# Kernel tuning notes

Hardware: AMD Instinct MI355X
Metric: run time of the kernel (lower is better)

The kernel has to match this reference:

```python
import jax, jax.numpy as jnp
import numpy as np

N = 50000        # n_nodes
E = 1600000      # n_edges (avg degree 32)
M = 8            # multiplicity of node irreps 8x0e + 8x1o
R = 8            # radial embedding dim
H = 8            # radial MLP hidden width
OUT_IRREPS = 6 * M   # 24x0e + 24x1o -> 48 irreps (MLP output width)
AVG_NEIGH = 32.0
SQRT3 = np.sqrt(3.0).astype(np.float32)


def setup_inputs() -> dict:
    key = jax.random.key(0)
    ks = jax.random.split(key, 7)
    node_feats = jax.random.normal(ks[0], (N, 4 * M), dtype=jnp.float32)      # [M scalars | M*3 vector comps]
    edge_features = jax.random.normal(ks[1], (E, 4), dtype=jnp.float32)       # SH l=0 (1) + l=1 (3)
    radial_embedding = jax.random.uniform(ks[2], (E, R), dtype=jnp.float32)
    senders = jax.random.randint(ks[3], (E,), 0, N, dtype=jnp.int32)
    receivers = jax.random.randint(ks[4], (E,), 0, N, dtype=jnp.int32)
    w1 = jax.random.normal(ks[5], (R, H), dtype=jnp.float32) / np.sqrt(R).astype(np.float32)
    w2 = jax.random.normal(ks[6], (H, OUT_IRREPS), dtype=jnp.float32) / np.sqrt(H).astype(np.float32)
    return {"node_feats": node_feats, "edge_features": edge_features,
            "radial_embedding": radial_embedding, "w1": w1, "w2": w2,
            "senders": senders, "receivers": receivers}


def reference(node_feats, edge_features, radial_embedding, w1, w2, senders, receivers):
    # 1) irregular gather: messages = node_feats[senders]
    msg = node_feats[senders]                       # [E, 4M]
    s = msg[:, :M]                                  # [E, M]   scalars (0e)
    v = msg[:, M:].reshape(-1, M, 3)                # [E, M, 3] vectors (1o)
    e0 = edge_features[:, :1]                       # [E, 1]   SH l=0
    e1 = edge_features[:, 1:4]                      # [E, 3]   SH l=1

    # 2) CG tensor product node x edge, filtered to irreps_out + '0e' (= 0e + 1o)
    tp0a = s * e0                                   # 0e x 0e -> 0e   [E, M]
    tp0b = jnp.einsum('emc,ec->em', v, e1) / SQRT3  # 1o x 1o -> 0e   [E, M]
    tp1a = s[:, :, None] * e1[:, None, :]           # 0e x 1o -> 1o   [E, M, 3]
    tp1b = v * e0[:, :, None]                       # 1o x 0e -> 1o   [E, M, 3]

    # 3) concatenate original (filtered) messages with tp output, regrouped: 3M x 0e + 3M x 1o
    scal = jnp.concatenate([s, tp0a, tp0b], axis=1)        # [E, 3M]
    vec = jnp.concatenate([v, tp1a, tp1b], axis=1)         # [E, 3M, 3]

    # 4) radial MLP (no bias, swish hidden, linear output) -> one weight per irrep
    w = jax.nn.swish(radial_embedding @ w1) @ w2           # [E, 6M]
    scal = scal * w[:, :3 * M]
    vec = vec * w[:, 3 * M:, None]                          # broadcast over 3 components

    messages = jnp.concatenate([scal, vec.reshape(vec.shape[0], -1)], axis=1)  # [E, 12M]

    # 5) scatter-add to receivers + neighbour normalization
    out = jax.ops.segment_sum(messages, receivers, num_segments=N)             # [N, 12M]
    return out / np.sqrt(AVG_NEIGH).astype(np.float32)
```

## Files before the change

### kernel.cpp

```cpp
#include <hip/hip_runtime.h>


#define CAPACITY 96
#define CH 16

typedef _Float16 half2v __attribute__((ext_vector_type(2)));

__device__ __forceinline__ unsigned pk16(float a, float b) {
    return __builtin_bit_cast(unsigned, __builtin_amdgcn_cvt_pkrtz(a, b));
}

__device__ __forceinline__ float dot2h(unsigned a, half2v b, float c) {
#if __has_builtin(__builtin_amdgcn_fdot2)
    return __builtin_amdgcn_fdot2(__builtin_bit_cast(half2v, a), b, c, false);
#else
    half2v av = __builtin_bit_cast(half2v, a);
    return fmaf((float)av.x, (float)b.x, fmaf((float)av.y, (float)b.y, c));
#endif
}

__global__ __launch_bounds__(256) void hist_kernel(
    const int* __restrict__ recv, int* __restrict__ cnt, int E)
{
    int e = blockIdx.x * 256 + threadIdx.x;
    if (e < E) atomicAdd(&cnt[recv[e]], 1);
}

__global__ __launch_bounds__(1024) void scan_kernel(
    const int* __restrict__ cnt, int* __restrict__ off,
    int* __restrict__ cursor, int N)
{
    __shared__ int lds[1024];
    const int t = threadIdx.x;
    const int CHN = (N + 1023) / 1024;
    const int lo = t * CHN;
    const int hi = min(N, lo + CHN);
    int s = 0;
    for (int i = lo; i < hi; ++i) s += cnt[i];
    lds[t] = s;
    __syncthreads();
    for (int d = 1; d < 1024; d <<= 1) {
        int v = (t >= d) ? lds[t - d] : 0;
        __syncthreads();
        lds[t] += v;
        __syncthreads();
    }
    int run = (t > 0) ? lds[t - 1] : 0;
    for (int i = lo; i < hi; ++i) {
        off[i] = run;
        cursor[i] = run;
        run += cnt[i];
    }
    if (t == 1023) off[N] = lds[1023];
}

__global__ __launch_bounds__(256) void build_recs_kernel(
    const float* __restrict__ edge_features,
    const float* __restrict__ radial,
    const float* __restrict__ w1g,
    const int* __restrict__ senders,
    const int* __restrict__ recv,
    int* __restrict__ slots,
    uint4* __restrict__ recs,
    int E, int CAP)
{
    __shared__ float sw1[64];
    for (int i = threadIdx.x; i < 64; i += 256) sw1[i] = w1g[i];
    __syncthreads();

    int e = blockIdx.x * 256 + threadIdx.x;
    if (e >= E) return;

    const int rcv_ = recv[e];
    size_t addr;
    if (CAP > 0) {
        int slot = atomicAdd(&slots[rcv_], 1);
        slot = min(slot, CAP - 1);
        addr = (size_t)rcv_ * CAP + slot;
    } else {
        addr = (size_t)atomicAdd(&slots[rcv_], 1);
    }

    const float4 ef = reinterpret_cast<const float4*>(edge_features)[e];
    const float4 ra = reinterpret_cast<const float4*>(radial)[2 * e + 0];
    const float4 rb = reinterpret_cast<const float4*>(radial)[2 * e + 1];
    const int snd = senders[e];

    float r[8] = {ra.x, ra.y, ra.z, ra.w, rb.x, rb.y, rb.z, rb.w};
    float h[8];
#pragma unroll
    for (int j = 0; j < 8; ++j) {
        float x = 0.f;
#pragma unroll
        for (int i = 0; i < 8; ++i) x = fmaf(r[i], sw1[i * 8 + j], x);
        h[j] = 0.17677669529663687f * x * __builtin_amdgcn_rcpf(1.0f + __expf(-x));
    }

    uint4 qa, qb;
    qa.x = pk16(h[0], h[1]); qa.y = pk16(h[2], h[3]);
    qa.z = pk16(h[4], h[5]); qa.w = pk16(h[6], h[7]);
    qb.x = pk16(ef.x, ef.y); qb.y = pk16(ef.z, ef.w);
    qb.z = (unsigned)snd;    qb.w = 0u;
    recs[2 * addr + 0] = qa;
    recs[2 * addr + 1] = qb;
}

__device__ __forceinline__ void comp_params(int c, int& k, int& i0, int& sel, int& t2)
{
    if (c < 8)       { k = c;      i0 = c;           sel = 0; t2 = 0; }
    else if (c < 16) { int m = c - 8;  k = 8 + m;  i0 = m;         sel = 1; t2 = 0; }
    else if (c < 24) { int m = c - 16; k = 16 + m; i0 = 8 + 3 * m; sel = 2; t2 = 1; }
    else if (c < 48) { int m = (c - 24) / 3, x = (c - 24) % 3;
                       k = 24 + m; i0 = 8 + 3 * m + x; sel = 0;     t2 = 0; }
    else if (c < 72) { int m = (c - 48) / 3, x = (c - 48) % 3;
                       k = 32 + m; i0 = m;             sel = 2 + x; t2 = 0; }
    else             { int m = (c - 72) / 3, x = (c - 72) % 3;
                       k = 40 + m; i0 = 8 + 3 * m + x; sel = 1;     t2 = 0; }
}

template<bool CAPMODE>
__global__ __launch_bounds__(256) void node_v10_kernel(
    const float* __restrict__ node_feats,
    const float* __restrict__ w2g,
    const int* __restrict__ off,
    const uint4* __restrict__ recs,
    float* __restrict__ out,
    int N)
{
    const int lane = threadIdx.x & 63;
    const int wv   = threadIdx.x >> 6;
    const int node = blockIdx.x * 4 + wv;

    __shared__ uint4 rec_lds[4][CH][2];
    __shared__ float nf_lds[4][CH][32];

    int k0, i0a, sel0, t20;
    int k1, i1a, sel1, t21;
    comp_params(lane, k0, i0a, sel0, t20);
    comp_params(64 + (lane & 31), k1, i1a, sel1, t21);
    const int i0b = t20 ? i0a + 1 : i0a;
    const int i0c = t20 ? i0a + 2 : i0a;

    const float inv_sqrt3 = 0.57735026918962576f;
    const float sc0 = t20 ? inv_sqrt3 : 1.0f;
    half2v wp0[4], wp1[4];
#pragma unroll
    for (int i = 0; i < 4; ++i) {
        wp0[i].x = (_Float16)(w2g[(2 * i + 0) * 48 + k0] * sc0);
        wp0[i].y = (_Float16)(w2g[(2 * i + 1) * 48 + k0] * sc0);
        wp1[i].x = (_Float16)(w2g[(2 * i + 0) * 48 + k1]);
        wp1[i].y = (_Float16)(w2g[(2 * i + 1) * 48 + k1]);
    }

    if (node >= N) return;

    int base, count;
    if (CAPMODE) { base = node * CAPACITY; count = min(off[node], CAPACITY); }
    else         { base = off[node];       count = off[node + 1] - base; }
    const uint4* rp = recs + (size_t)base * 2;

    const int r_stage = lane >> 2;
    const int q_stage = lane & 3;

    float acc0 = 0.f, acc1 = 0.f;

    for (int c0i = 0; c0i < count; c0i += CH) {
        const int cc = min(CH, count - c0i);

        if (lane < 2 * cc)
            rec_lds[wv][lane >> 1][lane & 1] = rp[(size_t)c0i * 2 + lane];

        if (r_stage < cc) {
            const unsigned snd = rec_lds[wv][r_stage][1].z;
            const float4* src = reinterpret_cast<const float4*>(node_feats)
                                + (size_t)snd * 8 + q_stage * 2;
            const float4 v0 = src[0];
            const float4 v1 = src[1];
            float4* dst = reinterpret_cast<float4*>(&nf_lds[wv][r_stage][q_stage * 8]);
            dst[0] = v0;
            dst[1] = v1;
        }

        for (int i = 0; i < cc; ++i) {
            const uint4 qa = rec_lds[wv][i][0];
            const uint4 qb = rec_lds[wv][i][1];

            float wA = dot2h(qa.x, wp0[0], 0.f);
            wA = dot2h(qa.y, wp0[1], wA);
            wA = dot2h(qa.z, wp0[2], wA);
            wA = dot2h(qa.w, wp0[3], wA);
            float wB = dot2h(qa.x, wp1[0], 0.f);
            wB = dot2h(qa.y, wp1[1], wB);
            wB = dot2h(qa.z, wp1[2], wB);
            wB = dot2h(qa.w, wp1[3], wB);

            const half2v eA = __builtin_bit_cast(half2v, qb.x);
            const half2v eB = __builtin_bit_cast(half2v, qb.y);
            const float e0  = (float)eA.x, e1x = (float)eA.y;
            const float e1y = (float)eB.x, e1z = (float)eB.y;

            const float n00 = nf_lds[wv][i][i0a];
            const float n01 = nf_lds[wv][i][i0b];
            const float n02 = nf_lds[wv][i][i0c];
            const float n10 = nf_lds[wv][i][i1a];

            const float f00 = (sel0 == 0) ? 1.0f
                            : (sel0 == 1) ? e0
                            : (sel0 == 2) ? e1x
                            : (sel0 == 3) ? e1y : e1z;
            const float f01 = t20 ? e1y : 0.0f;
            const float f02 = t20 ? e1z : 0.0f;
            acc0 = fmaf(wA, fmaf(n02, f02, fmaf(n01, f01, n00 * f00)), acc0);

            const float f10 = (sel1 == 1) ? e0
                            : (sel1 == 2) ? e1x
                            : (sel1 == 3) ? e1y : e1z;
            acc1 = fmaf(wB, n10 * f10, acc1);
        }
    }

    float* orow = out + (size_t)node * 96;
    orow[lane] = acc0;
    if (lane < 32) orow[64 + lane] = acc1;
}

extern "C" void kernel_launch(void* const* d_in, const int* in_sizes, int n_in,
                              void* d_out, int out_size, void* d_ws, size_t ws_size,
                              hipStream_t stream) {
    const float* node_feats    = (const float*)d_in[0];
    const float* edge_features = (const float*)d_in[1];
    const float* radial        = (const float*)d_in[2];
    const float* w1            = (const float*)d_in[3];
    const float* w2            = (const float*)d_in[4];
    const int*   senders       = (const int*)d_in[5];
    const int*   receivers     = (const int*)d_in[6];
    float* out = (float*)d_out;

    const int E = in_sizes[5];
    const int N = out_size / 96;
    const int eblocks = (E + 255) / 256;
    const int nblocks = (N + 3) / 4;

    const size_t needP1 = (size_t)N * CAPACITY * 32 + (size_t)N * sizeof(int);

    if (ws_size >= needP1) {
        uint4* recs = (uint4*)d_ws;
        int* cnt = (int*)((char*)d_ws + (size_t)N * CAPACITY * 32);

        (void)hipMemsetAsync(cnt, 0, (size_t)N * sizeof(int), stream);
        hipLaunchKernelGGL(build_recs_kernel, dim3(eblocks), dim3(256), 0, stream,
                           edge_features, radial, w1, senders, receivers,
                           cnt, recs, E, CAPACITY);
        hipLaunchKernelGGL(node_v10_kernel<true>, dim3(nblocks), dim3(256), 0, stream,
                           node_feats, w2, cnt, recs, out, N);
    } else {
        uint4* recs = (uint4*)d_ws;
        int* cnt    = (int*)((char*)d_ws + (size_t)E * 32);
        int* off    = cnt + N;
        int* cursor = cnt + 2 * N + 1;

        (void)hipMemsetAsync(cnt, 0, (size_t)N * sizeof(int), stream);
        hipLaunchKernelGGL(hist_kernel, dim3(eblocks), dim3(256), 0, stream,
                           receivers, cnt, E);
        hipLaunchKernelGGL(scan_kernel, dim3(1), dim3(1024), 0, stream,
                           cnt, off, cursor, N);
        hipLaunchKernelGGL(build_recs_kernel, dim3(eblocks), dim3(256), 0, stream,
                           edge_features, radial, w1, senders, receivers,
                           cursor, recs, E, 0);
        hipLaunchKernelGGL(node_v10_kernel<false>, dim3(nblocks), dim3(256), 0, stream,
                           node_feats, w2, off, recs, out, N);
    }
}
```

Before: 321.5 us.

## Replace LDS chunk staging with register-prefetched per-edge loop in node kernel

The node kernel no longer stages edge records and sender rows through LDS in chunks of 16. Each lane now reads records straight from global memory with a two-deep register prefetch, and reads its sender feature element with a wave-uniform address from readfirstlane. Lane roles are remapped so each lane handles one scalar product term, and the three-term 1o·1o dot product is reduced through a small LDS scratch at the end. This removes the LDS staging and the barrier-free chunk overhead, but every lane now issues redundant broadcast global loads and the loop becomes latency-bound per edge.

```diff
diff --git a/kernel.cpp b/kernel.cpp
--- a/kernel.cpp
+++ b/kernel.cpp
@@ -2,7 +2,6 @@
 
 
 #define CAPACITY 96
-#define CH 16
 
 typedef _Float16 half2v __attribute__((ext_vector_type(2)));
 
@@ -105,21 +104,8 @@
     recs[2 * addr + 1] = qb;
 }
 
-__device__ __forceinline__ void comp_params(int c, int& k, int& i0, int& sel, int& t2)
-{
-    if (c < 8)       { k = c;      i0 = c;           sel = 0; t2 = 0; }
-    else if (c < 16) { int m = c - 8;  k = 8 + m;  i0 = m;         sel = 1; t2 = 0; }
-    else if (c < 24) { int m = c - 16; k = 16 + m; i0 = 8 + 3 * m; sel = 2; t2 = 1; }
-    else if (c < 48) { int m = (c - 24) / 3, x = (c - 24) % 3;
-                       k = 24 + m; i0 = 8 + 3 * m + x; sel = 0;     t2 = 0; }
-    else if (c < 72) { int m = (c - 48) / 3, x = (c - 48) % 3;
-                       k = 32 + m; i0 = m;             sel = 2 + x; t2 = 0; }
-    else             { int m = (c - 72) / 3, x = (c - 72) % 3;
-                       k = 40 + m; i0 = 8 + 3 * m + x; sel = 1;     t2 = 0; }
-}
-
 template<bool CAPMODE>
-__global__ __launch_bounds__(256) void node_v10_kernel(
+__global__ __launch_bounds__(256) void node_v11_kernel(
     const float* __restrict__ node_feats,
     const float* __restrict__ w2g,
     const int* __restrict__ off,
@@ -131,25 +117,27 @@
     const int wv   = threadIdx.x >> 6;
     const int node = blockIdx.x * 4 + wv;
 
-    __shared__ uint4 rec_lds[4][CH][2];
-    __shared__ float nf_lds[4][CH][32];
-
-    int k0, i0a, sel0, t20;
-    int k1, i1a, sel1, t21;
-    comp_params(lane, k0, i0a, sel0, t20);
-    comp_params(64 + (lane & 31), k1, i1a, sel1, t21);
-    const int i0b = t20 ? i0a + 1 : i0a;
-    const int i0c = t20 ? i0a + 2 : i0a;
-
-    const float inv_sqrt3 = 0.57735026918962576f;
-    const float sc0 = t20 ? inv_sqrt3 : 1.0f;
-    half2v wp0[4], wp1[4];
+    __shared__ float scr[4][128];
+
+    int kA, iA, selA; float scA = 1.0f;
+    if (lane < 8)       { kA = lane;         iA = lane;     selA = 0; }
+    else if (lane < 16) { kA = lane;         iA = lane - 8; selA = 1; }
+    else if (lane < 40) { int t = lane - 16; kA = 16 + t / 3; iA = 8 + t;
+                          selA = 2 + t % 3;  scA = 0.57735026918962576f; }
+    else                { int t = lane - 40; kA = 24 + t / 3; iA = 8 + t; selA = 0; }
+
+    int kB, iB, selB; const bool deadB = (lane >= 48);
+    if (lane < 24)      { int t = lane;      kB = 32 + t / 3; iB = t / 3; selB = 2 + t % 3; }
+    else if (lane < 48) { int t = lane - 24; kB = 40 + t / 3; iB = 8 + t; selB = 1; }
+    else                { kB = 0; iB = 0; selB = 0; }
+
+    half2v wpA[4], wpB[4];
 #pragma unroll
     for (int i = 0; i < 4; ++i) {
-        wp0[i].x = (_Float16)(w2g[(2 * i + 0) * 48 + k0] * sc0);
-        wp0[i].y = (_Float16)(w2g[(2 * i + 1) * 48 + k0] * sc0);
-        wp1[i].x = (_Float16)(w2g[(2 * i + 0) * 48 + k1]);
-        wp1[i].y = (_Float16)(w2g[(2 * i + 1) * 48 + k1]);
+        wpA[i].x = (_Float16)(w2g[(2 * i + 0) * 48 + kA] * scA);
+        wpA[i].y = (_Float16)(w2g[(2 * i + 1) * 48 + kA] * scA);
+        wpB[i].x = deadB ? (_Float16)0.f : (_Float16)(w2g[(2 * i + 0) * 48 + kB]);
+        wpB[i].y = deadB ? (_Float16)0.f : (_Float16)(w2g[(2 * i + 1) * 48 + kB]);
     }
 
     if (node >= N) return;
@@ -157,71 +145,76 @@
     int base, count;
     if (CAPMODE) { base = node * CAPACITY; count = min(off[node], CAPACITY); }
     else         { base = off[node];       count = off[node + 1] - base; }
+    base  = __builtin_amdgcn_readfirstlane(base);
+    count = __builtin_amdgcn_readfirstlane(count);
     const uint4* rp = recs + (size_t)base * 2;
 
-    const int r_stage = lane >> 2;
-    const int q_stage = lane & 3;
-
     float acc0 = 0.f, acc1 = 0.f;
-
-    for (int c0i = 0; c0i < count; c0i += CH) {
-        const int cc = min(CH, count - c0i);
-
-        if (lane < 2 * cc)
-            rec_lds[wv][lane >> 1][lane & 1] = rp[(size_t)c0i * 2 + lane];
-
-        if (r_stage < cc) {
-            const unsigned snd = rec_lds[wv][r_stage][1].z;
-            const float4* src = reinterpret_cast<const float4*>(node_feats)
-                                + (size_t)snd * 8 + q_stage * 2;
-            const float4 v0 = src[0];
-            const float4 v1 = src[1];
-            float4* dst = reinterpret_cast<float4*>(&nf_lds[wv][r_stage][q_stage * 8]);
-            dst[0] = v0;
-            dst[1] = v1;
-        }
-
-        for (int i = 0; i < cc; ++i) {
-            const uint4 qa = rec_lds[wv][i][0];
-            const uint4 qb = rec_lds[wv][i][1];
-
-            float wA = dot2h(qa.x, wp0[0], 0.f);
-            wA = dot2h(qa.y, wp0[1], wA);
-            wA = dot2h(qa.z, wp0[2], wA);
-            wA = dot2h(qa.w, wp0[3], wA);
-            float wB = dot2h(qa.x, wp1[0], 0.f);
-            wB = dot2h(qa.y, wp1[1], wB);
-            wB = dot2h(qa.z, wp1[2], wB);
-            wB = dot2h(qa.w, wp1[3], wB);
-
-            const half2v eA = __builtin_bit_cast(half2v, qb.x);
-            const half2v eB = __builtin_bit_cast(half2v, qb.y);
+    if (count > 0) {
+        const int last = count - 1;
+        uint4 qaC = rp[0], qbC = rp[1];
+        const int j1 = min(1, last), j2 = min(2, last);
+        uint4 qaN1 = rp[2 * j1], qbN1 = rp[2 * j1 + 1];
+        uint4 qaN2 = rp[2 * j2], qbN2 = rp[2 * j2 + 1];
+        int snd0 = __builtin_amdgcn_readfirstlane((int)qbC.z);
+        const float* row0 = node_feats + (size_t)snd0 * 32;
+        float n0 = row0[iA];
+        float n1 = row0[iB];
+
+#pragma unroll 2
+        for (int i = 0; i < count; ++i) {
+            const int sndN = __builtin_amdgcn_readfirstlane((int)qbN1.z);
+            const float* rowN = node_feats + (size_t)sndN * 32;
+            const float n0N = rowN[iA];
+            const float n1N = rowN[iB];
+
+            float wAv = dot2h(qaC.x, wpA[0], 0.f);
+            wAv = dot2h(qaC.y, wpA[1], wAv);
+            wAv = dot2h(qaC.z, wpA[2], wAv);
+            wAv = dot2h(qaC.w, wpA[3], wAv);
+            float wBv = dot2h(qaC.x, wpB[0], 0.f);
+            wBv = dot2h(qaC.y, wpB[1], wBv);
+            wBv = dot2h(qaC.z, wpB[2], wBv);
+            wBv = dot2h(qaC.w, wpB[3], wBv);
+
+            const half2v eA = __builtin_bit_cast(half2v, qbC.x);
+            const half2v eB = __builtin_bit_cast(half2v, qbC.y);
             const float e0  = (float)eA.x, e1x = (float)eA.y;
             const float e1y = (float)eB.x, e1z = (float)eB.y;
 
-            const float n00 = nf_lds[wv][i][i0a];
-            const float n01 = nf_lds[wv][i][i0b];
-            const float n02 = nf_lds[wv][i][i0c];
-            const float n10 = nf_lds[wv][i][i1a];
-
-            const float f00 = (sel0 == 0) ? 1.0f
-                            : (sel0 == 1) ? e0
-                            : (sel0 == 2) ? e1x
-                            : (sel0 == 3) ? e1y : e1z;
-            const float f01 = t20 ? e1y : 0.0f;
-            const float f02 = t20 ? e1z : 0.0f;
-            acc0 = fmaf(wA, fmaf(n02, f02, fmaf(n01, f01, n00 * f00)), acc0);
-
-            const float f10 = (sel1 == 1) ? e0
-                            : (sel1 == 2) ? e1x
-                            : (sel1 == 3) ? e1y : e1z;
-            acc1 = fmaf(wB, n10 * f10, acc1);
+            const float fA = (selA == 0) ? 1.0f
+                           : (selA == 1) ? e0
+                           : (selA == 2) ? e1x
+                           : (selA == 3) ? e1y : e1z;
+            const float fB = (selB == 1) ? e0
+                           : (selB == 2) ? e1x
+                           : (selB == 3) ? e1y : e1z;
+
+            acc0 = fmaf(wAv, n0 * fA, acc0);
+            acc1 = fmaf(wBv, n1 * fB, acc1);
+
+            qaC = qaN1; qbC = qbN1;
+            qaN1 = qaN2; qbN1 = qbN2;
+            n0 = n0N; n1 = n1N;
+            const int jp = min(i + 3, last);
+            qaN2 = rp[2 * jp]; qbN2 = rp[2 * jp + 1];
         }
     }
 
+    scr[wv][lane]      = acc0;
+    scr[wv][64 + lane] = acc1;
+    float o0;
+    if (lane < 16) {
+        o0 = scr[wv][lane];
+    } else if (lane < 24) {
+        const int t = 16 + 3 * (lane - 16);
+        o0 = scr[wv][t] + scr[wv][t + 1] + scr[wv][t + 2];
+    } else {
+        o0 = scr[wv][lane + 16];
+    }
     float* orow = out + (size_t)node * 96;
-    orow[lane] = acc0;
-    if (lane < 32) orow[64 + lane] = acc1;
+    orow[lane] = o0;
+    if (lane < 32) orow[64 + lane] = scr[wv][80 + lane];
 }
 
 extern "C" void kernel_launch(void* const* d_in, const int* in_sizes, int n_in,
@@ -251,7 +244,7 @@
         hipLaunchKernelGGL(build_recs_kernel, dim3(eblocks), dim3(256), 0, stream,
                            edge_features, radial, w1, senders, receivers,
                            cnt, recs, E, CAPACITY);
-        hipLaunchKernelGGL(node_v10_kernel<true>, dim3(nblocks), dim3(256), 0, stream,
+        hipLaunchKernelGGL(node_v11_kernel<true>, dim3(nblocks), dim3(256), 0, stream,
                            node_feats, w2, cnt, recs, out, N);
     } else {
         uint4* recs = (uint4*)d_ws;
@@ -267,7 +260,7 @@
         hipLaunchKernelGGL(build_recs_kernel, dim3(eblocks), dim3(256), 0, stream,
                            edge_features, radial, w1, senders, receivers,
                            cursor, recs, E, 0);
-        hipLaunchKernelGGL(node_v10_kernel<false>, dim3(nblocks), dim3(256), 0, stream,
+        hipLaunchKernelGGL(node_v11_kernel<false>, dim3(nblocks), dim3(256), 0, stream,
                            node_feats, w2, off, recs, out, N);
     }
 }
```

Result: slower. 362.0 us (+12.6%).
